# Kernel tuning notes

Measured on AMD Instinct MI355X. Metric: run time of the kernel, lower is better.

The kernel has to match this reference:

```python
import jax, jax.numpy as jnp
import numpy as np

# Static problem sizes (see shape_source)
B, SX, SY = 256, 256, 70          # graphs, encoder nodes/graph, decoder nodes/graph
F, EMB, H = 512, 256, 256          # f_size, emb_size, h_size
VOCAB = 256
E = 4 * B * SY                     # 71680 edges
N_SLT = 4                          # SltEdgeTypes
N_SRT = 8                          # len(SrtEdgeTypes)


def setup_inputs() -> dict:
    key = jax.random.key(0)
    ks = jax.random.split(key, 24)
    s = 0.02
    inp = {
        'x': jax.random.normal(ks[0], (B * SX, F), jnp.float32),
        'x_batch': jnp.repeat(jnp.arange(B, dtype=jnp.int64), SX),
        'tgt_y': jax.random.randint(ks[1], (B * SY,), 0, VOCAB, jnp.int64),
        'tgt_edge_index': jax.random.randint(ks[2], (2, E), 0, B * SY, jnp.int64),
        'tgt_edge_type': jax.random.randint(ks[3], (E,), 0, N_SLT, jnp.int64),
        'tgt_y_batch': jnp.repeat(jnp.arange(B, dtype=jnp.int64), SY),
        'embeds': jax.random.normal(ks[4], (VOCAB, EMB), jnp.float32) * s,
    }
    dims = [(EMB, H), (H, H), (H, EMB)]
    k = 5
    for l, (din, dout) in enumerate(dims, start=1):
        inp[f'W_in{l}'] = jax.random.normal(ks[k + 0], (din, dout), jnp.float32) * s
        inp[f'Wq{l}'] = jax.random.normal(ks[k + 1], (dout, F), jnp.float32) * s
        inp[f'Wv{l}'] = jax.random.normal(ks[k + 2], (F, dout), jnp.float32) * s
        inp[f'Ee{l}'] = jax.random.normal(ks[k + 3], (N_SLT, dout), jnp.float32) * s
        k += 4
    inp['lin_z_w'] = jax.random.normal(ks[k], (EMB, VOCAB), jnp.float32) * s
    inp['lin_z_b'] = jnp.zeros((VOCAB,), jnp.float32)
    inp['lin_g_w'] = jax.random.normal(ks[k + 1], (2 * EMB, N_SRT), jnp.float32) * s
    inp['lin_g_b'] = jnp.zeros((N_SRT,), jnp.float32)
    return inp


def gcn_dec_layer(x_b, y, src, tgt, etype, W_in, Wq, Wv, Ee):
    """Edge-type-conditioned message passing + cross-attention onto encoder x.
    x_b: [B,SX,F]; y: [Ny,din]. Returns ([Ny,dout], alpha [B,SY,SX])."""
    h = y @ W_in                                   # [Ny, dout]
    m = h[src] + Ee[etype]                         # gather + type embedding
    agg = jax.ops.segment_sum(m, tgt, num_segments=y.shape[0])
    q = (h @ Wq).reshape(B, SY, F)                 # query into encoder space
    logits = jnp.einsum('bqf,bkf->bqk', q, x_b) / jnp.sqrt(jnp.float32(F))
    alpha = jax.nn.softmax(logits, axis=-1)        # [B,SY,SX]
    ctx = jnp.einsum('bqk,bkf->bqf', alpha, x_b) @ Wv  # [B,SY,dout]
    out = jax.nn.relu(h + agg + ctx.reshape(h.shape[0], -1))
    return out, alpha


def reference(x, x_batch, tgt_y, tgt_edge_index, tgt_edge_type, tgt_y_batch,
              embeds, W_in1, Wq1, Wv1, Ee1, W_in2, Wq2, Wv2, Ee2,
              W_in3, Wq3, Wv3, Ee3, lin_z_w, lin_z_b, lin_g_w, lin_g_b):
    x_b = x.reshape(B, SX, F)
    src, tgt = tgt_edge_index[0], tgt_edge_index[1]
    y = embeds[tgt_y]                              # [Ny, EMB]
    y, a1 = gcn_dec_layer(x_b, y, src, tgt, tgt_edge_type, W_in1, Wq1, Wv1, Ee1)
    y, a2 = gcn_dec_layer(x_b, y, src, tgt, tgt_edge_type, W_in2, Wq2, Wv2, Ee2)
    y, a3 = gcn_dec_layer(x_b, y, src, tgt, tgt_edge_type, W_in3, Wq3, Wv3, Ee3)
    y_score = y @ lin_z_w + lin_z_b                # [Ny, VOCAB]
    ef = y[tgt_edge_index]                         # [2, E, EMB]
    ef = jnp.transpose(ef, (1, 0, 2)).reshape(E, 2 * EMB)
    y_edge_rel_score = ef @ lin_g_w + lin_g_b      # [E, N_SRT]
    return (y, y_score, y_edge_rel_score, a1, a2, a3)
```

## Files before the change

### kernel.cpp

```cpp
#include <hip/hip_runtime.h>
#include <cstddef>
#include <cstdint>

#define B_    256
#define SX_   256
#define SY_   70
#define F_    512
#define EMB_  256
#define NY_   (B_*SY_)
#define NE_   (4*B_*SY_)

typedef short s16x8 __attribute__((ext_vector_type(8)));
typedef float f32x4 __attribute__((ext_vector_type(4)));
typedef unsigned short us4 __attribute__((ext_vector_type(4)));
typedef unsigned short us8 __attribute__((ext_vector_type(8)));

__device__ __forceinline__ unsigned short f2bf(float f) {
    unsigned u = __builtin_bit_cast(unsigned, f);
    u += 0x7fffu + ((u >> 16) & 1u);
    return (unsigned short)(u >> 16);
}
__device__ __forceinline__ float bf2f(unsigned short b) {
    unsigned u = ((unsigned)b) << 16;
    return __builtin_bit_cast(float, u);
}

template<int EPI, int SWZ>
__global__ __launch_bounds__(256, 2)
void gemm_mfma(const unsigned short* __restrict__ A, int lda, long sAb,
               const unsigned short* __restrict__ Bt, int ldb, long sBb,
               float* __restrict__ Cf, int ldc, long sCfb,
               unsigned short* __restrict__ Cb, int ldcb, long sCbb,
               const float* __restrict__ aux1, long sAux,
               int M, int K, float scale, int nx, int ny)
{
    __shared__ unsigned short As[128 * 64];
    __shared__ unsigned short Bs[128 * 64];
    char* AsB = (char*)As;
    char* BsB = (char*)Bs;
    const int tid = threadIdx.x;
    int bxi, byi, z;
    if (SWZ) {
        const int nwg = gridDim.x;
        const int bid = blockIdx.x;
        const int wg = (bid & 7) * (nwg >> 3) + (bid >> 3);
        bxi = wg % nx;
        byi = (wg / nx) % ny;
        z   = wg / (nx * ny);
    } else {
        bxi = blockIdx.x; byi = blockIdx.y; z = blockIdx.z;
    }
    A  += (size_t)z * sAb;
    Bt += (size_t)z * sBb;
    const char* auxp = (const char*)aux1 + (size_t)z * sAux;
    const int bm = byi * 128, bn = bxi * 128;
    const int lane = tid & 63;
    const int w = tid >> 6, wr = w >> 1, wc = w & 1;
    const int l15 = lane & 15, lq = lane >> 4;

    f32x4 acc[4][4];
    const f32x4 z4 = {0.f, 0.f, 0.f, 0.f};
#pragma unroll
    for (int m = 0; m < 4; ++m)
#pragma unroll
        for (int n = 0; n < 4; ++n) acc[m][n] = z4;

    for (int k0 = 0; k0 < K; k0 += 64) {
#pragma unroll
        for (int i = 0; i < 4; ++i) {
            const int row = i * 32 + (tid >> 3);
            const int k8  = (tid & 7) ^ (row & 7);
            int ra = bm + row; ra = (ra < M) ? ra : (M - 1);
            const unsigned short* g = A + (size_t)ra * lda + k0 + k8 * 8;
            __builtin_amdgcn_global_load_lds(
                (const __attribute__((address_space(1))) unsigned int*)g,
                (__attribute__((address_space(3))) unsigned int*)(AsB + i * 4096 + tid * 16),
                16, 0, 0);
        }
#pragma unroll
        for (int i = 0; i < 4; ++i) {
            const int row = i * 32 + (tid >> 3);
            const int k8  = (tid & 7) ^ (row & 7);
            const unsigned short* g = Bt + (size_t)(bn + row) * ldb + k0 + k8 * 8;
            __builtin_amdgcn_global_load_lds(
                (const __attribute__((address_space(1))) unsigned int*)g,
                (__attribute__((address_space(3))) unsigned int*)(BsB + i * 4096 + tid * 16),
                16, 0, 0);
        }
        __syncthreads();
#pragma unroll
        for (int kk = 0; kk < 2; ++kk) {
            s16x8 af[4], bf[4];
#pragma unroll
            for (int m = 0; m < 4; ++m) {
                const int row = wr * 64 + m * 16 + l15;
                const int slot = (kk * 4 + lq) ^ (row & 7);
                af[m] = *(const s16x8*)(AsB + row * 128 + slot * 16);
            }
#pragma unroll
            for (int n = 0; n < 4; ++n) {
                const int col = wc * 64 + n * 16 + l15;
                const int slot = (kk * 4 + lq) ^ (col & 7);
                bf[n] = *(const s16x8*)(BsB + col * 128 + slot * 16);
            }
#pragma unroll
            for (int m = 0; m < 4; ++m)
#pragma unroll
                for (int n = 0; n < 4; ++n)
                    acc[m][n] = __builtin_amdgcn_mfma_f32_16x16x32_bf16(
                        af[m], bf[n], acc[m][n], 0, 0, 0);
        }
        __syncthreads();
    }

    float* cf = Cf ? Cf + (size_t)z * sCfb : nullptr;
    unsigned short* cb = Cb ? Cb + (size_t)z * sCbb : nullptr;
#pragma unroll
    for (int m = 0; m < 4; ++m) {
#pragma unroll
        for (int n = 0; n < 4; ++n) {
            const int col = bn + wc * 64 + n * 16 + l15;
            f32x4 v = acc[m][n];
#pragma unroll
            for (int r = 0; r < 4; ++r) {
                const int gr = bm + wr * 64 + m * 16 + lq * 4 + r;
                if (gr >= M) continue;
                float o = v[r] * scale;
                if (EPI == 4) o += ((const float*)auxp)[col];
                if (EPI == 7) {
                    if (col < 256) cb[(size_t)gr * ldcb + col] = f2bf(o);
                    else ((unsigned short*)cf)[(size_t)gr * 512 + (col - 256)] = f2bf(o);
                } else {
                    if (cf) cf[(size_t)gr * ldc + col] = o;
                    if (cb) cb[(size_t)gr * ldcb + col] = f2bf(o);
                }
            }
        }
    }
}

template<int LAST>
__global__ __launch_bounds__(512, 1)
void attn_pv(const unsigned short* __restrict__ Q,
             const unsigned short* __restrict__ X,
             const unsigned short* __restrict__ XV,
             long sXVb,
             const unsigned short* __restrict__ aggb,
             const unsigned short* __restrict__ lzT,
             const float* __restrict__ lzb,
             const float* __restrict__ gw,
             float* __restrict__ Y12g,
             float* __restrict__ Aout,
             unsigned short* __restrict__ Yb,
             float* __restrict__ Yf,
             float* __restrict__ Score,
             float scale)
{
    __shared__ unsigned short SB[3 * 12288];
    __shared__ unsigned short Al[128 * 256];
    __shared__ float red[4][2][64];
    char* SBb = (char*)SB;
    char* AlB = (char*)Al;
    const int tid = threadIdx.x;
    const int z = blockIdx.x;
    const unsigned short* Qb  = Q + (size_t)z * SY_ * F_;
    const unsigned short* Xb  = X + (size_t)z * SX_ * F_;
    const unsigned short* xvb = XV + (size_t)z * sXVb;
    const int lane = tid & 63;
    const int w = tid >> 6, wr = w >> 2, wc = w & 3;
    const int l15 = lane & 15, lq = lane >> 4;

    auto stage1 = [&](int t) {
        char* base = SBb + (t % 3) * 24576;
        {
            const int row = tid >> 2;
            const int k8  = (tid & 3) ^ ((row >> 1) & 3);
            const int ra = (row < SY_) ? row : (SY_ - 1);
            const unsigned short* g = Qb + (size_t)ra * F_ + t * 32 + k8 * 8;
            __builtin_amdgcn_global_load_lds(
                (const __attribute__((address_space(1))) unsigned int*)g,
                (__attribute__((address_space(3))) unsigned int*)(base + tid * 16),
                16, 0, 0);
        }
#pragma unroll
        for (int i = 0; i < 2; ++i) {
            const int row = i * 128 + (tid >> 2);
            const int k8  = (tid & 3) ^ ((row >> 1) & 3);
            const unsigned short* g = Xb + (size_t)row * F_ + t * 32 + k8 * 8;
            __builtin_amdgcn_global_load_lds(
                (const __attribute__((address_space(1))) unsigned int*)g,
                (__attribute__((address_space(3))) unsigned int*)(base + 8192 + i * 8192 + tid * 16),
                16, 0, 0);
        }
    };

    f32x4 acc[4][4];
    const f32x4 z4 = {0.f, 0.f, 0.f, 0.f};
#pragma unroll
    for (int m = 0; m < 4; ++m)
#pragma unroll
        for (int n = 0; n < 4; ++n) acc[m][n] = z4;

    stage1(0);
    stage1(1);
    for (int t = 0; t < 16; ++t) {
        if (t + 2 < 16) stage1(t + 2);
        if (t < 14)       asm volatile("s_waitcnt vmcnt(6)" ::: "memory");
        else if (t == 14) asm volatile("s_waitcnt vmcnt(3)" ::: "memory");
        else              asm volatile("s_waitcnt vmcnt(0)" ::: "memory");
        __builtin_amdgcn_s_barrier();
        asm volatile("" ::: "memory");
        char* base = SBb + (t % 3) * 24576;
        s16x8 af[4], bf[4];
#pragma unroll
        for (int m = 0; m < 4; ++m) {
            const int row = wr * 64 + m * 16 + l15;
            const int slot = lq ^ ((row >> 1) & 3);
            af[m] = *(const s16x8*)(base + row * 64 + slot * 16);
        }
#pragma unroll
        for (int n = 0; n < 4; ++n) {
            const int col = wc * 64 + n * 16 + l15;
            const int slot = lq ^ ((col >> 1) & 3);
            bf[n] = *(const s16x8*)(base + 8192 + col * 64 + slot * 16);
        }
#pragma unroll
        for (int m = 0; m < 4; ++m)
#pragma unroll
            for (int n = 0; n < 4; ++n)
                acc[m][n] = __builtin_amdgcn_mfma_f32_16x16x32_bf16(
                    af[m], bf[n], acc[m][n], 0, 0, 0);
        asm volatile("" ::: "memory");
        __builtin_amdgcn_s_barrier();
    }

#pragma unroll
    for (int m = 0; m < 4; ++m)
#pragma unroll
        for (int n = 0; n < 4; ++n)
#pragma unroll
            for (int r = 0; r < 4; ++r) acc[m][n][r] *= scale;

    float rmax[4][4];
#pragma unroll
    for (int m = 0; m < 4; ++m)
#pragma unroll
        for (int r = 0; r < 4; ++r) {
            float mx = acc[m][0][r];
#pragma unroll
            for (int n = 1; n < 4; ++n) mx = fmaxf(mx, acc[m][n][r]);
            mx = fmaxf(mx, __shfl_xor(mx, 1));
            mx = fmaxf(mx, __shfl_xor(mx, 2));
            mx = fmaxf(mx, __shfl_xor(mx, 4));
            mx = fmaxf(mx, __shfl_xor(mx, 8));
            rmax[m][r] = mx;
        }
    if (l15 == 0) {
#pragma unroll
        for (int m = 0; m < 4; ++m)
#pragma unroll
            for (int r = 0; r < 4; ++r)
                red[wc][wr][m * 16 + lq * 4 + r] = rmax[m][r];
    }
    __syncthreads();
    float rtot[4][4];
#pragma unroll
    for (int m = 0; m < 4; ++m)
#pragma unroll
        for (int r = 0; r < 4; ++r) {
            const int lr = m * 16 + lq * 4 + r;
            rtot[m][r] = fmaxf(fmaxf(red[0][wr][lr], red[1][wr][lr]),
                               fmaxf(red[2][wr][lr], red[3][wr][lr]));
        }
    __syncthreads();
    float rsum[4][4];
#pragma unroll
    for (int m = 0; m < 4; ++m)
#pragma unroll
        for (int r = 0; r < 4; ++r) {
            float s = 0.f;
#pragma unroll
            for (int n = 0; n < 4; ++n) {
                float e = __expf(acc[m][n][r] - rtot[m][r]);
                acc[m][n][r] = e;
                s += e;
            }
            s += __shfl_xor(s, 1);
            s += __shfl_xor(s, 2);
            s += __shfl_xor(s, 4);
            s += __shfl_xor(s, 8);
            rsum[m][r] = s;
        }
    if (l15 == 0) {
#pragma unroll
        for (int m = 0; m < 4; ++m)
#pragma unroll
            for (int r = 0; r < 4; ++r)
                red[wc][wr][m * 16 + lq * 4 + r] = rsum[m][r];
    }
    __syncthreads();
#pragma unroll
    for (int m = 0; m < 4; ++m)
#pragma unroll
        for (int r = 0; r < 4; ++r) {
            const int lr = m * 16 + lq * 4 + r;
            const int row = wr * 64 + lr;
            const float inv = 1.0f / (red[0][wr][lr] + red[1][wr][lr] +
                                      red[2][wr][lr] + red[3][wr][lr]);
#pragma unroll
            for (int n = 0; n < 4; ++n) {
                const int col = wc * 64 + n * 16 + l15;
                *(unsigned short*)(AlB + row * 512 +
                    (((col >> 3) ^ (row & 7)) << 4) + ((col & 7) << 1))
                    = f2bf(acc[m][n][r] * inv);
            }
        }
    __syncthreads();
    {
        float* ao = Aout + (size_t)z * SY_ * SX_;
        for (int idx = tid; idx < SY_ * 8; idx += 512) {
            const int row = idx >> 3, seg = idx & 7;
            float tmp[32];
#pragma unroll
            for (int c8 = 0; c8 < 4; ++c8) {
                const int chunk = seg * 4 + c8;
                us8 v = *(const us8*)(AlB + row * 512 + ((chunk ^ (row & 7)) << 4));
#pragma unroll
                for (int j = 0; j < 8; ++j) tmp[c8 * 8 + j] = bf2f(v[j]);
            }
            float* dst = ao + (size_t)row * SX_ + seg * 32;
#pragma unroll
            for (int q = 0; q < 8; ++q) {
                float4 o4; o4.x = tmp[q*4]; o4.y = tmp[q*4+1];
                o4.z = tmp[q*4+2]; o4.w = tmp[q*4+3];
                ((float4*)dst)[q] = o4;
            }
        }
    }

    char* v_buf[2] = {SBb, SBb + 32768};
    auto stage2 = [&](int k0, int buf, const unsigned short* srcm) {
        char* bb = v_buf[buf];
#pragma unroll
        for (int i = 0; i < 4; ++i) {
            const int row = i * 64 + (tid >> 3);
            const int k8  = (tid & 7) ^ (row & 7);
            const unsigned short* g = srcm + (size_t)row * 256 + k0 + k8 * 8;
            __builtin_amdgcn_global_load_lds(
                (const __attribute__((address_space(1))) unsigned int*)g,
                (__attribute__((address_space(3))) unsigned int*)(bb + i * 8192 + tid * 16),
                16, 0, 0);
        }
    };

    f32x4 oac[4][4];
#pragma unroll
    for (int m = 0; m < 4; ++m)
#pragma unroll
        for (int n = 0; n < 4; ++n) oac[m][n] = z4;

    stage2(0, 0, xvb);
    __syncthreads();
    int cur = 0;
    for (int ks = 0; ks < 4; ++ks) {
        if (ks < 3) stage2((ks + 1) * 64, cur ^ 1, xvb);
        char* bb = v_buf[cur];
        const int k0 = ks * 64;
#pragma unroll
        for (int kk = 0; kk < 2; ++kk) {
            s16x8 af[4], bf[4];
#pragma unroll
            for (int m = 0; m < 4; ++m) {
                const int row = wr * 64 + m * 16 + l15;
                const int chunk = (k0 >> 3) + kk * 4 + lq;
                af[m] = *(const s16x8*)(AlB + row * 512 + ((chunk ^ (row & 7)) << 4));
            }
#pragma unroll
            for (int n = 0; n < 4; ++n) {
                const int col = wc * 64 + n * 16 + l15;
                const int slot = (kk * 4 + lq) ^ (col & 7);
                bf[n] = *(const s16x8*)(bb + col * 128 + slot * 16);
            }
#pragma unroll
            for (int m = 0; m < 4; ++m)
#pragma unroll
                for (int n = 0; n < 4; ++n)
                    oac[m][n] = __builtin_amdgcn_mfma_f32_16x16x32_bf16(
                        af[m], bf[n], oac[m][n], 0, 0, 0);
        }
        __syncthreads();
        cur ^= 1;
    }

#pragma unroll
    for (int m = 0; m < 4; ++m)
#pragma unroll
        for (int n = 0; n < 4; ++n) {
            const int col = wc * 64 + n * 16 + l15;
            f32x4 v = oac[m][n];
#pragma unroll
            for (int r = 0; r < 4; ++r) {
                const int row = wr * 64 + m * 16 + lq * 4 + r;
                if (row >= SY_) continue;
                *(unsigned short*)(AlB + row * 512 +
                    (((col >> 3) ^ (row & 7)) << 4) + ((col & 7) << 1)) = f2bf(v[r]);
            }
        }
    __syncthreads();
    {
        const size_t nodeBase = (size_t)z * SY_;
        for (int idx = tid; idx < SY_ * 8; idx += 512) {
            const int row = idx >> 3, seg = idx & 7;
            const size_t node = nodeBase + row;
            float tmp[32];
#pragma unroll
            for (int c8 = 0; c8 < 4; ++c8) {
                const int chunk = seg * 4 + c8;
                us8 ov = *(const us8*)(AlB + row * 512 + ((chunk ^ (row & 7)) << 4));
                us8 av = *(const us8*)(aggb + node * 256 + seg * 32 + c8 * 8);
                us8 o;
#pragma unroll
                for (int j = 0; j < 8; ++j) {
                    float val = fmaxf(bf2f(ov[j]) + bf2f(av[j]), 0.f);
                    tmp[c8 * 8 + j] = val;
                    o[j] = f2bf(val);
                }
                *(us8*)(Yb + node * 256 + seg * 32 + c8 * 8) = o;
                if (LAST)
                    *(us8*)(AlB + row * 512 + ((chunk ^ (row & 7)) << 4)) = o;
            }
            if (Yf) {
                float* dst = Yf + node * 256 + seg * 32;
#pragma unroll
                for (int q = 0; q < 8; ++q) {
                    float4 o4; o4.x = tmp[q*4]; o4.y = tmp[q*4+1];
                    o4.z = tmp[q*4+2]; o4.w = tmp[q*4+3];
                    ((float4*)dst)[q] = o4;
                }
            }
        }
    }

    if (LAST) {
        __syncthreads();
#pragma unroll
        for (int m = 0; m < 4; ++m)
#pragma unroll
            for (int n = 0; n < 4; ++n) oac[m][n] = z4;
        stage2(0, 0, lzT);
        __syncthreads();
        cur = 0;
        for (int ks = 0; ks < 4; ++ks) {
            if (ks < 3) stage2((ks + 1) * 64, cur ^ 1, lzT);
            char* bb = v_buf[cur];
            const int k0 = ks * 64;
#pragma unroll
            for (int kk = 0; kk < 2; ++kk) {
                s16x8 af[4], bf[4];
#pragma unroll
                for (int m = 0; m < 4; ++m) {
                    const int row = wr * 64 + m * 16 + l15;
                    const int chunk = (k0 >> 3) + kk * 4 + lq;
                    af[m] = *(const s16x8*)(AlB + row * 512 + ((chunk ^ (row & 7)) << 4));
                }
#pragma unroll
                for (int n = 0; n < 4; ++n) {
                    const int col = wc * 64 + n * 16 + l15;
                    const int slot = (kk * 4 + lq) ^ (col & 7);
                    bf[n] = *(const s16x8*)(bb + col * 128 + slot * 16);
                }
#pragma unroll
                for (int m = 0; m < 4; ++m)
#pragma unroll
                    for (int n = 0; n < 4; ++n)
                        oac[m][n] = __builtin_amdgcn_mfma_f32_16x16x32_bf16(
                            af[m], bf[n], oac[m][n], 0, 0, 0);
            }
            __syncthreads();
            cur ^= 1;
        }
#pragma unroll
        for (int m = 0; m < 4; ++m)
#pragma unroll
            for (int n = 0; n < 4; ++n) {
                const int col = wc * 64 + n * 16 + l15;
                f32x4 v = oac[m][n];
#pragma unroll
                for (int r = 0; r < 4; ++r) {
                    const int row = wr * 64 + m * 16 + lq * 4 + r;
                    if (row >= SY_) continue;
                    Score[((size_t)z * SY_ + row) * 256 + col] = v[r] + lzb[col];
                }
            }

        __syncthreads();
        float* Ws = (float*)SBb;
        for (int i = tid; i < 1024; i += 512)
            ((float4*)Ws)[i] = ((const float4*)gw)[i];
        __syncthreads();
        for (int t = tid; t < 1120; t += 512) {
            const int row = t >> 4, j = t & 15;
            const float* Wcol = Ws + ((j < 8) ? j : (2048 + j - 8));
            float a2 = 0.f;
            for (int c = 0; c < 256; ++c) {
                const float yv = bf2f(*(const unsigned short*)(AlB + row * 512 +
                    (((c >> 3) ^ (row & 7)) << 4) + ((c & 7) << 1)));
                a2 = fmaf(yv, Wcol[c * 8], a2);
            }
            Y12g[((size_t)z * SY_ + row) * 16 + j] = a2;
        }
    }
}

__global__ __launch_bounds__(256)
void conv_x_embed(const float* __restrict__ in, unsigned short* __restrict__ out,
                  int n8, const float* __restrict__ embeds,
                  const int* __restrict__ tgt_y, unsigned short* __restrict__ yb)
{
    if (blockIdx.x < 2048) {
        for (int i = blockIdx.x * 256 + threadIdx.x; i < n8; i += 2048 * 256) {
            float4 a = ((const float4*)in)[i * 2];
            float4 b = ((const float4*)in)[i * 2 + 1];
            us8 o = { f2bf(a.x), f2bf(a.y), f2bf(a.z), f2bf(a.w),
                      f2bf(b.x), f2bf(b.y), f2bf(b.z), f2bf(b.w) };
            ((us8*)out)[i] = o;
        }
    } else {
        const int i = (blockIdx.x - 2048) * 8 + (threadIdx.x >> 5);
        const int c8 = (threadIdx.x & 31) * 8;
        const int v = tgt_y[i];
        const float* p = embeds + (size_t)v * 256 + c8;
        float4 a = *(const float4*)p;
        float4 b = *(const float4*)(p + 4);
        us8 o = { f2bf(a.x), f2bf(a.y), f2bf(a.z), f2bf(a.w),
                  f2bf(b.x), f2bf(b.y), f2bf(b.z), f2bf(b.w) };
        *(us8*)(yb + (size_t)i * 256 + c8) = o;
    }
}

struct WAll {
    const float* src[10];
    unsigned short* dst[10];
    int R[10];
    int C[10];
};

__global__ __launch_bounds__(256)
void conv_wT_all(WAll d)
{
    const int z = blockIdx.z;
    const int R = d.R[z], C = d.C[z];
    const int c0 = blockIdx.x * 64, r0 = blockIdx.y * 64;
    if (c0 >= C || r0 >= R) return;
    const float* in = d.src[z];
    unsigned short* outT = d.dst[z];
    __shared__ unsigned short t[64][65];
    const int r = threadIdx.x >> 4, cq = (threadIdx.x & 15) << 2;
#pragma unroll
    for (int i = 0; i < 4; ++i) {
        const int rr = r + i * 16;
        float4 v = *(const float4*)(in + (size_t)(r0 + rr) * C + c0 + cq);
        t[rr][cq + 0] = f2bf(v.x); t[rr][cq + 1] = f2bf(v.y);
        t[rr][cq + 2] = f2bf(v.z); t[rr][cq + 3] = f2bf(v.w);
    }
    __syncthreads();
    const int c = threadIdx.x >> 2, sq = (threadIdx.x & 3) << 4;
    us8 o0, o1;
#pragma unroll
    for (int i = 0; i < 8; ++i) { o0[i] = t[sq + i][c]; o1[i] = t[sq + 8 + i][c]; }
    *(us8*)(outT + (size_t)(c0 + c) * R + r0 + sq) = o0;
    *(us8*)(outT + (size_t)(c0 + c) * R + r0 + sq + 8) = o1;
}

__global__ __launch_bounds__(256)
void edge_deg(const int* __restrict__ tgt, int* __restrict__ deg)
{
    const int e = blockIdx.x * 256 + threadIdx.x;
    if (e < NE_) atomicAdd(&deg[tgt[e]], 1);
}

__global__ __launch_bounds__(1024)
void scan_off(const int* __restrict__ deg, int* __restrict__ off, int* __restrict__ cursor)
{
    __shared__ int ls[1024];
    const int t = threadIdx.x;
    const int base = t * 18;
    int local[18];
    int s = 0;
#pragma unroll
    for (int i = 0; i < 18; ++i) {
        const int idx = base + i;
        const int v = (idx < NY_) ? deg[idx] : 0;
        local[i] = s; s += v;
    }
    ls[t] = s;
    __syncthreads();
    for (int d = 1; d < 1024; d <<= 1) {
        int v = (t >= d) ? ls[t - d] : 0;
        __syncthreads();
        ls[t] += v;
        __syncthreads();
    }
    const int excl = (t == 0) ? 0 : ls[t - 1];
#pragma unroll
    for (int i = 0; i < 18; ++i) {
        const int idx = base + i;
        if (idx < NY_) {
            const int o = excl + local[i];
            off[idx] = o; cursor[idx] = o;
        }
    }
    if (t == 1023) off[NY_] = ls[1023];
}

__global__ __launch_bounds__(256)
void edge_fill(const int* __restrict__ tgt, int* __restrict__ cursor,
               int* __restrict__ elist)
{
    const int e = blockIdx.x * 256 + threadIdx.x;
    if (e >= NE_) return;
    const int pos = atomicAdd(&cursor[tgt[e]], 1);
    elist[pos] = e;
}

__global__ __launch_bounds__(256)
void node_agg(const unsigned short* __restrict__ hb,
              const float* __restrict__ Ee,
              const int* __restrict__ src, const int* __restrict__ etype,
              const int* __restrict__ off, const int* __restrict__ elist,
              unsigned short* __restrict__ aggb)
{
    const int nid  = blockIdx.x * 4 + (threadIdx.x >> 6);
    const int lane = threadIdx.x & 63;
    const int c = lane * 4;
    const int k0 = off[nid], k1 = off[nid + 1];
    us4 sv = *(const us4*)(hb + (size_t)nid * 256 + c);
    float4 acc;
    acc.x = bf2f(sv[0]); acc.y = bf2f(sv[1]);
    acc.z = bf2f(sv[2]); acc.w = bf2f(sv[3]);
    int cnt0 = 0, cnt1 = 0, cnt2 = 0, cnt3 = 0;
    for (int k = k0; k < k1; ++k) {
        const int e = elist[k];
        const int sfrom = src[e];
        const int ty = etype[e];
        us4 hv = *(const us4*)(hb + (size_t)sfrom * 256 + c);
        acc.x += bf2f(hv[0]); acc.y += bf2f(hv[1]);
        acc.z += bf2f(hv[2]); acc.w += bf2f(hv[3]);
        cnt0 += (ty == 0); cnt1 += (ty == 1); cnt2 += (ty == 2); cnt3 += (ty == 3);
    }
    float4 e0 = *(const float4*)(Ee + c);
    float4 e1 = *(const float4*)(Ee + 256 + c);
    float4 e2 = *(const float4*)(Ee + 512 + c);
    float4 e3 = *(const float4*)(Ee + 768 + c);
    acc.x += cnt0 * e0.x + cnt1 * e1.x + cnt2 * e2.x + cnt3 * e3.x;
    acc.y += cnt0 * e0.y + cnt1 * e1.y + cnt2 * e2.y + cnt3 * e3.y;
    acc.z += cnt0 * e0.z + cnt1 * e1.z + cnt2 * e2.z + cnt3 * e3.z;
    acc.w += cnt0 * e0.w + cnt1 * e1.w + cnt2 * e2.w + cnt3 * e3.w;
    us4 o = { f2bf(acc.x), f2bf(acc.y), f2bf(acc.z), f2bf(acc.w) };
    *(us4*)(aggb + (size_t)nid * 256 + c) = o;
}

__global__ __launch_bounds__(256)
void edge_gather(const float* __restrict__ Y12, const int* __restrict__ src,
                 const int* __restrict__ tgt, const float* __restrict__ bias,
                 float* __restrict__ esc)
{
    const int e = blockIdx.x * 256 + threadIdx.x;
    if (e >= NE_) return;
    const float* a = Y12 + (size_t)src[e] * 16;
    const float* b = Y12 + (size_t)tgt[e] * 16 + 8;
    float4 a0 = ((const float4*)a)[0], a1 = ((const float4*)a)[1];
    float4 b0 = ((const float4*)b)[0], b1 = ((const float4*)b)[1];
    float4 c0 = ((const float4*)bias)[0], c1 = ((const float4*)bias)[1];
    float4 o0, o1;
    o0.x = a0.x + b0.x + c0.x; o0.y = a0.y + b0.y + c0.y;
    o0.z = a0.z + b0.z + c0.z; o0.w = a0.w + b0.w + c0.w;
    o1.x = a1.x + b1.x + c1.x; o1.y = a1.y + b1.y + c1.y;
    o1.z = a1.z + b1.z + c1.z; o1.w = a1.w + b1.w + c1.w;
    ((float4*)(esc + (size_t)e * 8))[0] = o0;
    ((float4*)(esc + (size_t)e * 8))[1] = o1;
}

extern "C" void kernel_launch(void* const* d_in, const int* in_sizes, int n_in,
                              void* d_out, int out_size, void* d_ws, size_t ws_size,
                              hipStream_t stream)
{
    const float* x       = (const float*)d_in[0];
    const int*   tgt_y   = (const int*)d_in[2];
    const int*   eidx    = (const int*)d_in[3];
    const int*   etype   = (const int*)d_in[4];
    const float* embeds  = (const float*)d_in[6];
    const float* W_in[3] = {(const float*)d_in[7],  (const float*)d_in[11], (const float*)d_in[15]};
    const float* Wq[3]   = {(const float*)d_in[8],  (const float*)d_in[12], (const float*)d_in[16]};
    const float* Wv[3]   = {(const float*)d_in[9],  (const float*)d_in[13], (const float*)d_in[17]};
    const float* Ee[3]   = {(const float*)d_in[10], (const float*)d_in[14], (const float*)d_in[18]};
    const float* lin_z_w = (const float*)d_in[19];
    const float* lin_z_b = (const float*)d_in[20];
    const float* lin_g_w = (const float*)d_in[21];
    const float* lin_g_b = (const float*)d_in[22];
    const int* src = eidx;
    const int* tgt = eidx + NE_;

    float* out = (float*)d_out;
    float* y_final = out;
    float* score   = out + 4587520;
    float* esc     = out + 9175040;
    float* aout[3] = {out + 9748480, out + 14336000, out + 18923520};

    char* wsb = (char*)d_ws;
    unsigned short* xb     = (unsigned short*)(wsb + 0);
    unsigned short* xvTall = (unsigned short*)(wsb + 67108864);
    unsigned short* hb     = (unsigned short*)(wsb + 167772160);
    unsigned short* aggb   = (unsigned short*)(wsb + 176947200);
    unsigned short* qb     = (unsigned short*)(wsb + 186122240);
    unsigned short* yb     = (unsigned short*)(wsb + 204472320);
    char* wt = wsb + 213647360;
    unsigned short* wcatT[3], *wqT[3], *wvT[3];
    for (int l = 0; l < 3; ++l) {
        wcatT[l] = (unsigned short*)(wt + l * 393216);
        wqT[l]   = (unsigned short*)(wt + 1179648 + l * 262144);
        wvT[l]   = (unsigned short*)(wt + 1966080 + l * 262144);
    }
    unsigned short* lzT = (unsigned short*)(wt + 2752512);
    char* extra = wsb + 216530944;
    float* Y12    = (float*)extra;
    int*   deg    = (int*)(extra + 1146880);
    int*   off    = (int*)(extra + 1218560);
    int*   cursor = (int*)(extra + 1290244);
    int*   elist  = (int*)(extra + 1361924);

    hipMemsetAsync(deg, 0, NY_ * sizeof(int), stream);
    edge_deg<<<280, 256, 0, stream>>>(tgt, deg);
    scan_off<<<1, 1024, 0, stream>>>(deg, off, cursor);
    edge_fill<<<280, 256, 0, stream>>>(tgt, cursor, elist);

    conv_x_embed<<<4288, 256, 0, stream>>>(x, xb, 4194304, embeds, tgt_y, yb);
    WAll wd;
    for (int l = 0; l < 3; ++l) {
        wd.src[l]     = W_in[l]; wd.dst[l]     = wcatT[l]; wd.R[l]     = 256; wd.C[l]     = 256;
        wd.src[3 + l] = Wq[l];   wd.dst[3 + l] = wqT[l];   wd.R[3 + l] = 256; wd.C[3 + l] = 512;
        wd.src[6 + l] = Wv[l];   wd.dst[6 + l] = wvT[l];   wd.R[6 + l] = 512; wd.C[6 + l] = 256;
    }
    wd.src[9] = lin_z_w; wd.dst[9] = lzT; wd.R[9] = 256; wd.C[9] = 256;
    conv_wT_all<<<dim3(8, 8, 10), 256, 0, stream>>>(wd);

    gemm_mfma<0, 0><<<dim3(2, 4, 3), 256, 0, stream>>>(
        wqT[0], 256, 131072L,  wcatT[0], 256, 196608L,
        nullptr, 0, 0,  wcatT[0] + 65536, 256, 196608L,
        nullptr, 0, 512, 256, 1.f, 0, 0);

    gemm_mfma<0, 1><<<3072, 256, 0, stream>>>(
        wvT[0], 512, 0,  xb, 512, (long)SX_ * F_,
        nullptr, 0, 0,  xvTall, 256, 768L * 256,
        nullptr, 0, 768, 512, 1.f, 2, 6);

    const float qscale = 0.044194173824159216f;
    for (int l = 0; l < 3; ++l) {
        gemm_mfma<7, 0><<<dim3(6, 140, 1), 256, 0, stream>>>(
            yb, 256, 0,  wcatT[l], 256, 0,
            (float*)qb, 512, 0,  hb, 256, 0,
            nullptr, 0, NY_, 256, 1.f, 0, 0);
        node_agg<<<4480, 256, 0, stream>>>(hb, Ee[l], src, etype, off, elist, aggb);
        if (l < 2) {
            attn_pv<0><<<256, 512, 0, stream>>>(
                qb, xb, xvTall + (size_t)l * 65536, 768L * 256,
                aggb, nullptr, nullptr, nullptr, nullptr,
                aout[l], yb, nullptr, nullptr, qscale);
        } else {
            attn_pv<1><<<256, 512, 0, stream>>>(
                qb, xb, xvTall + (size_t)l * 65536, 768L * 256,
                aggb, lzT, lin_z_b, lin_g_w, Y12,
                aout[l], yb, y_final, score, qscale);
        }
    }
    edge_gather<<<280, 256, 0, stream>>>(Y12, src, tgt, lin_g_b, esc);
}
```

Measured before the change: 419.5 us.

## Precompute x·Wqᵀ per graph so attention logits contract over hidden dim

Reassociates the attention logits: instead of computing q = h·Wq (width 512) and contracting q against x over F=512, it precomputes XQ = x·Wqᵀ for all three layers once (a batched GEMM) and contracts h against XQ over 256. This halves the K loop in the attention kernel and removes the per-layer q projection from the node GEMM. The cost is a large extra up-front GEMM over all encoder nodes and a larger workspace buffer that the attention kernel reads.

```diff
diff --git a/kernel.cpp b/kernel.cpp
--- a/kernel.cpp
+++ b/kernel.cpp
@@ -25,13 +25,12 @@
     return __builtin_bit_cast(float, u);
 }
 
-template<int EPI, int SWZ>
+template<int SWZ>
 __global__ __launch_bounds__(256, 2)
 void gemm_mfma(const unsigned short* __restrict__ A, int lda, long sAb,
                const unsigned short* __restrict__ Bt, int ldb, long sBb,
                float* __restrict__ Cf, int ldc, long sCfb,
                unsigned short* __restrict__ Cb, int ldcb, long sCbb,
-               const float* __restrict__ aux1, long sAux,
                int M, int K, float scale, int nx, int ny)
 {
     __shared__ unsigned short As[128 * 64];
@@ -52,7 +51,6 @@
     }
     A  += (size_t)z * sAb;
     Bt += (size_t)z * sBb;
-    const char* auxp = (const char*)aux1 + (size_t)z * sAux;
     const int bm = byi * 128, bn = bxi * 128;
     const int lane = tid & 63;
     const int w = tid >> 6, wr = w >> 1, wc = w & 1;
@@ -126,14 +124,8 @@
                 const int gr = bm + wr * 64 + m * 16 + lq * 4 + r;
                 if (gr >= M) continue;
                 float o = v[r] * scale;
-                if (EPI == 4) o += ((const float*)auxp)[col];
-                if (EPI == 7) {
-                    if (col < 256) cb[(size_t)gr * ldcb + col] = f2bf(o);
-                    else ((unsigned short*)cf)[(size_t)gr * 512 + (col - 256)] = f2bf(o);
-                } else {
-                    if (cf) cf[(size_t)gr * ldc + col] = o;
-                    if (cb) cb[(size_t)gr * ldcb + col] = f2bf(o);
-                }
+                if (cf) cf[(size_t)gr * ldc + col] = o;
+                if (cb) cb[(size_t)gr * ldcb + col] = f2bf(o);
             }
         }
     }
@@ -141,8 +133,8 @@
 
 template<int LAST>
 __global__ __launch_bounds__(512, 1)
-void attn_pv(const unsigned short* __restrict__ Q,
-             const unsigned short* __restrict__ X,
+void attn_pv(const unsigned short* __restrict__ Hb,
+             const unsigned short* __restrict__ XQ,
              const unsigned short* __restrict__ XV,
              long sXVb,
              const unsigned short* __restrict__ aggb,
@@ -163,8 +155,8 @@
     char* AlB = (char*)Al;
     const int tid = threadIdx.x;
     const int z = blockIdx.x;
-    const unsigned short* Qb  = Q + (size_t)z * SY_ * F_;
-    const unsigned short* Xb  = X + (size_t)z * SX_ * F_;
+    const unsigned short* hbz = Hb + (size_t)z * SY_ * 256;
+    const unsigned short* xqz = XQ + (size_t)z * 196608;
     const unsigned short* xvb = XV + (size_t)z * sXVb;
     const int lane = tid & 63;
     const int w = tid >> 6, wr = w >> 2, wc = w & 3;
@@ -176,7 +168,7 @@
             const int row = tid >> 2;
             const int k8  = (tid & 3) ^ ((row >> 1) & 3);
             const int ra = (row < SY_) ? row : (SY_ - 1);
-            const unsigned short* g = Qb + (size_t)ra * F_ + t * 32 + k8 * 8;
+            const unsigned short* g = hbz + (size_t)ra * 256 + t * 32 + k8 * 8;
             __builtin_amdgcn_global_load_lds(
                 (const __attribute__((address_space(1))) unsigned int*)g,
                 (__attribute__((address_space(3))) unsigned int*)(base + tid * 16),
@@ -186,7 +178,7 @@
         for (int i = 0; i < 2; ++i) {
             const int row = i * 128 + (tid >> 2);
             const int k8  = (tid & 3) ^ ((row >> 1) & 3);
-            const unsigned short* g = Xb + (size_t)row * F_ + t * 32 + k8 * 8;
+            const unsigned short* g = xqz + (size_t)row * 768 + t * 32 + k8 * 8;
             __builtin_amdgcn_global_load_lds(
                 (const __attribute__((address_space(1))) unsigned int*)g,
                 (__attribute__((address_space(3))) unsigned int*)(base + 8192 + i * 8192 + tid * 16),
@@ -203,11 +195,11 @@
 
     stage1(0);
     stage1(1);
-    for (int t = 0; t < 16; ++t) {
-        if (t + 2 < 16) stage1(t + 2);
-        if (t < 14)       asm volatile("s_waitcnt vmcnt(6)" ::: "memory");
-        else if (t == 14) asm volatile("s_waitcnt vmcnt(3)" ::: "memory");
-        else              asm volatile("s_waitcnt vmcnt(0)" ::: "memory");
+    for (int t = 0; t < 8; ++t) {
+        if (t + 2 < 8) stage1(t + 2);
+        if (t < 6)       asm volatile("s_waitcnt vmcnt(6)" ::: "memory");
+        else if (t == 6) asm volatile("s_waitcnt vmcnt(3)" ::: "memory");
+        else             asm volatile("s_waitcnt vmcnt(0)" ::: "memory");
         __builtin_amdgcn_s_barrier();
         asm volatile("" ::: "memory");
         char* base = SBb + (t % 3) * 24576;
@@ -515,7 +507,9 @@
 __global__ __launch_bounds__(256)
 void conv_x_embed(const float* __restrict__ in, unsigned short* __restrict__ out,
                   int n8, const float* __restrict__ embeds,
-                  const int* __restrict__ tgt_y, unsigned short* __restrict__ yb)
+                  const int* __restrict__ tgt_y, unsigned short* __restrict__ yb,
+                  const float* __restrict__ wq1, const float* __restrict__ wq2,
+                  const float* __restrict__ wq3, unsigned short* __restrict__ wqcat)
 {
     if (blockIdx.x < 2048) {
         for (int i = blockIdx.x * 256 + threadIdx.x; i < n8; i += 2048 * 256) {
@@ -525,7 +519,7 @@
                       f2bf(b.x), f2bf(b.y), f2bf(b.z), f2bf(b.w) };
             ((us8*)out)[i] = o;
         }
-    } else {
+    } else if (blockIdx.x < 4288) {
         const int i = (blockIdx.x - 2048) * 8 + (threadIdx.x >> 5);
         const int c8 = (threadIdx.x & 31) * 8;
         const int v = tgt_y[i];
@@ -535,20 +529,31 @@
         us8 o = { f2bf(a.x), f2bf(a.y), f2bf(a.z), f2bf(a.w),
                   f2bf(b.x), f2bf(b.y), f2bf(b.z), f2bf(b.w) };
         *(us8*)(yb + (size_t)i * 256 + c8) = o;
+    } else {
+        const int idx = blockIdx.x - 4288;
+        const int which = idx >> 6;
+        const int i = (idx & 63) * 256 + threadIdx.x;
+        const float* src = (which == 0) ? wq1 : (which == 1) ? wq2 : wq3;
+        float4 a = ((const float4*)src)[i * 2];
+        float4 b = ((const float4*)src)[i * 2 + 1];
+        us8 o = { f2bf(a.x), f2bf(a.y), f2bf(a.z), f2bf(a.w),
+                  f2bf(b.x), f2bf(b.y), f2bf(b.z), f2bf(b.w) };
+        ((us8*)(wqcat + (size_t)which * 131072))[i] = o;
     }
 }
 
 struct WAll {
-    const float* src[10];
-    unsigned short* dst[10];
-    int R[10];
-    int C[10];
+    const float* src[8];
+    unsigned short* dst[8];
+    int R[8];
+    int C[8];
 };
 
 __global__ __launch_bounds__(256)
 void conv_wT_all(WAll d)
 {
     const int z = blockIdx.z;
+    if (z >= 7) return;
     const int R = d.R[z], C = d.C[z];
     const int c0 = blockIdx.x * 64, r0 = blockIdx.y * 64;
     if (c0 >= C || r0 >= R) return;
@@ -710,19 +715,19 @@
     char* wsb = (char*)d_ws;
     unsigned short* xb     = (unsigned short*)(wsb + 0);
     unsigned short* xvTall = (unsigned short*)(wsb + 67108864);
-    unsigned short* hb     = (unsigned short*)(wsb + 167772160);
-    unsigned short* aggb   = (unsigned short*)(wsb + 176947200);
-    unsigned short* qb     = (unsigned short*)(wsb + 186122240);
-    unsigned short* yb     = (unsigned short*)(wsb + 204472320);
-    char* wt = wsb + 213647360;
-    unsigned short* wcatT[3], *wqT[3], *wvT[3];
+    unsigned short* xqTall = (unsigned short*)(wsb + 167772160);
+    unsigned short* hb     = (unsigned short*)(wsb + 268435456);
+    unsigned short* aggb   = (unsigned short*)(wsb + 277610496);
+    unsigned short* yb     = (unsigned short*)(wsb + 286785536);
+    char* wt = wsb + 295960576;
+    unsigned short* winT[3], *wqT[3], *wvT[3];
     for (int l = 0; l < 3; ++l) {
-        wcatT[l] = (unsigned short*)(wt + l * 393216);
-        wqT[l]   = (unsigned short*)(wt + 1179648 + l * 262144);
-        wvT[l]   = (unsigned short*)(wt + 1966080 + l * 262144);
-    }
-    unsigned short* lzT = (unsigned short*)(wt + 2752512);
-    char* extra = wsb + 216530944;
+        winT[l] = (unsigned short*)(wt + l * 131072);
+        wqT[l]  = (unsigned short*)(wt + 393216  + l * 262144);
+        wvT[l]  = (unsigned short*)(wt + 1179648 + l * 262144);
+    }
+    unsigned short* lzT = (unsigned short*)(wt + 1966080);
+    char* extra = wsb + 298057728;
     float* Y12    = (float*)extra;
     int*   deg    = (int*)(extra + 1146880);
     int*   off    = (int*)(extra + 1218560);
@@ -734,41 +739,42 @@
     scan_off<<<1, 1024, 0, stream>>>(deg, off, cursor);
     edge_fill<<<280, 256, 0, stream>>>(tgt, cursor, elist);
 
-    conv_x_embed<<<4288, 256, 0, stream>>>(x, xb, 4194304, embeds, tgt_y, yb);
+    conv_x_embed<<<4480, 256, 0, stream>>>(x, xb, 4194304, embeds, tgt_y, yb,
+                                           Wq[0], Wq[1], Wq[2], wqT[0]);
     WAll wd;
     for (int l = 0; l < 3; ++l) {
-        wd.src[l]     = W_in[l]; wd.dst[l]     = wcatT[l]; wd.R[l]     = 256; wd.C[l]     = 256;
-        wd.src[3 + l] = Wq[l];   wd.dst[3 + l] = wqT[l];   wd.R[3 + l] = 256; wd.C[3 + l] = 512;
-        wd.src[6 + l] = Wv[l];   wd.dst[6 + l] = wvT[l];   wd.R[6 + l] = 512; wd.C[6 + l] = 256;
-    }
-    wd.src[9] = lin_z_w; wd.dst[9] = lzT; wd.R[9] = 256; wd.C[9] = 256;
-    conv_wT_all<<<dim3(8, 8, 10), 256, 0, stream>>>(wd);
-
-    gemm_mfma<0, 0><<<dim3(2, 4, 3), 256, 0, stream>>>(
-        wqT[0], 256, 131072L,  wcatT[0], 256, 196608L,
-        nullptr, 0, 0,  wcatT[0] + 65536, 256, 196608L,
-        nullptr, 0, 512, 256, 1.f, 0, 0);
-
-    gemm_mfma<0, 1><<<3072, 256, 0, stream>>>(
+        wd.src[l]     = W_in[l]; wd.dst[l]     = winT[l]; wd.R[l]     = 256; wd.C[l]     = 256;
+        wd.src[3 + l] = Wv[l];   wd.dst[3 + l] = wvT[l];  wd.R[3 + l] = 512; wd.C[3 + l] = 256;
+    }
+    wd.src[6] = lin_z_w; wd.dst[6] = lzT; wd.R[6] = 256; wd.C[6] = 256;
+    wd.src[7] = lin_z_w; wd.dst[7] = lzT; wd.R[7] = 0; wd.C[7] = 0;
+    conv_wT_all<<<dim3(8, 8, 7), 256, 0, stream>>>(wd);
+
+    gemm_mfma<1><<<3072, 256, 0, stream>>>(
         wvT[0], 512, 0,  xb, 512, (long)SX_ * F_,
         nullptr, 0, 0,  xvTall, 256, 768L * 256,
-        nullptr, 0, 768, 512, 1.f, 2, 6);
+        768, 512, 1.f, 2, 6);
+
+    gemm_mfma<1><<<3072, 256, 0, stream>>>(
+        xb, 512, (long)SX_ * F_,  wqT[0], 512, 0,
+        nullptr, 0, 0,  xqTall, 768, 256L * 768,
+        256, 512, 1.f, 6, 2);
 
     const float qscale = 0.044194173824159216f;
     for (int l = 0; l < 3; ++l) {
-        gemm_mfma<7, 0><<<dim3(6, 140, 1), 256, 0, stream>>>(
-            yb, 256, 0,  wcatT[l], 256, 0,
-            (float*)qb, 512, 0,  hb, 256, 0,
-            nullptr, 0, NY_, 256, 1.f, 0, 0);
+        gemm_mfma<0><<<dim3(2, 140, 1), 256, 0, stream>>>(
+            yb, 256, 0,  winT[l], 256, 0,
+            nullptr, 0, 0,  hb, 256, 0,
+            NY_, 256, 1.f, 0, 0);
         node_agg<<<4480, 256, 0, stream>>>(hb, Ee[l], src, etype, off, elist, aggb);
         if (l < 2) {
             attn_pv<0><<<256, 512, 0, stream>>>(
-                qb, xb, xvTall + (size_t)l * 65536, 768L * 256,
+                hb, xqTall + (size_t)l * 256, xvTall + (size_t)l * 65536, 768L * 256,
                 aggb, nullptr, nullptr, nullptr, nullptr,
                 aout[l], yb, nullptr, nullptr, qscale);
         } else {
             attn_pv<1><<<256, 512, 0, stream>>>(
-                qb, xb, xvTall + (size_t)l * 65536, 768L * 256,
+                hb, xqTall + (size_t)l * 256, xvTall + (size_t)l * 65536, 768L * 256,
                 aggb, lzT, lin_z_b, lin_g_w, Y12,
                 aout[l], yb, y_final, score, qscale);
         }
```

New measurement: 446.2 us. +6.4%, slower.

## Split attention kernel into two half-query blocks per graph with smaller LDS

Applied to the files above, without the earlier changes.

The attention/PV kernel now launches two 256-thread blocks per graph, each handling 35 of the 70 query rows, instead of one 512-thread block handling all 70 padded to 128. This drops the padding waste from 128 to 64 rows per block (still padded from 35) and shrinks LDS use so two blocks can share a CU, raising occupancy and the grid to 512 blocks. In exchange, each block reloads the full X and XV tiles, doubling that global traffic. The pipeline also becomes simpler and shallower: QK moves from triple buffering to double buffering, and the PV and score loops lose their prefetch, so they load then sync each step. An unused aux epilogue parameter is removed from the GEMM.

```diff
diff --git a/kernel.cpp b/kernel.cpp
--- a/kernel.cpp
+++ b/kernel.cpp
@@ -31,7 +31,6 @@
                const unsigned short* __restrict__ Bt, int ldb, long sBb,
                float* __restrict__ Cf, int ldc, long sCfb,
                unsigned short* __restrict__ Cb, int ldcb, long sCbb,
-               const float* __restrict__ aux1, long sAux,
                int M, int K, float scale, int nx, int ny)
 {
     __shared__ unsigned short As[128 * 64];
@@ -52,7 +51,6 @@
     }
     A  += (size_t)z * sAb;
     Bt += (size_t)z * sBb;
-    const char* auxp = (const char*)aux1 + (size_t)z * sAux;
     const int bm = byi * 128, bn = bxi * 128;
     const int lane = tid & 63;
     const int w = tid >> 6, wr = w >> 1, wc = w & 1;
@@ -126,7 +124,6 @@
                 const int gr = bm + wr * 64 + m * 16 + lq * 4 + r;
                 if (gr >= M) continue;
                 float o = v[r] * scale;
-                if (EPI == 4) o += ((const float*)auxp)[col];
                 if (EPI == 7) {
                     if (col < 256) cb[(size_t)gr * ldcb + col] = f2bf(o);
                     else ((unsigned short*)cf)[(size_t)gr * 512 + (col - 256)] = f2bf(o);
@@ -140,7 +137,7 @@
 }
 
 template<int LAST>
-__global__ __launch_bounds__(512, 1)
+__global__ __launch_bounds__(256, 2)
 void attn_pv(const unsigned short* __restrict__ Q,
              const unsigned short* __restrict__ X,
              const unsigned short* __restrict__ XV,
@@ -156,40 +153,41 @@
              float* __restrict__ Score,
              float scale)
 {
-    __shared__ unsigned short SB[3 * 12288];
-    __shared__ unsigned short Al[128 * 256];
-    __shared__ float red[4][2][64];
+    __shared__ unsigned short SB[2 * 10240];
+    __shared__ unsigned short Al[64 * 256];
+    __shared__ float red[4][64];
     char* SBb = (char*)SB;
     char* AlB = (char*)Al;
     const int tid = threadIdx.x;
-    const int z = blockIdx.x;
+    const int z  = blockIdx.x >> 1;
+    const int h0 = (blockIdx.x & 1) * 35;
     const unsigned short* Qb  = Q + (size_t)z * SY_ * F_;
     const unsigned short* Xb  = X + (size_t)z * SX_ * F_;
     const unsigned short* xvb = XV + (size_t)z * sXVb;
     const int lane = tid & 63;
-    const int w = tid >> 6, wr = w >> 2, wc = w & 3;
+    const int wc = tid >> 6;
     const int l15 = lane & 15, lq = lane >> 4;
 
-    auto stage1 = [&](int t) {
-        char* base = SBb + (t % 3) * 24576;
+    auto stage1 = [&](int t, int buf) {
+        char* base = SBb + buf * 20480;
         {
             const int row = tid >> 2;
             const int k8  = (tid & 3) ^ ((row >> 1) & 3);
-            const int ra = (row < SY_) ? row : (SY_ - 1);
-            const unsigned short* g = Qb + (size_t)ra * F_ + t * 32 + k8 * 8;
+            const int rl  = (row < 35) ? row : 34;
+            const unsigned short* g = Qb + (size_t)(h0 + rl) * F_ + t * 32 + k8 * 8;
             __builtin_amdgcn_global_load_lds(
                 (const __attribute__((address_space(1))) unsigned int*)g,
                 (__attribute__((address_space(3))) unsigned int*)(base + tid * 16),
                 16, 0, 0);
         }
 #pragma unroll
-        for (int i = 0; i < 2; ++i) {
-            const int row = i * 128 + (tid >> 2);
+        for (int i = 0; i < 4; ++i) {
+            const int row = i * 64 + (tid >> 2);
             const int k8  = (tid & 3) ^ ((row >> 1) & 3);
             const unsigned short* g = Xb + (size_t)row * F_ + t * 32 + k8 * 8;
             __builtin_amdgcn_global_load_lds(
                 (const __attribute__((address_space(1))) unsigned int*)g,
-                (__attribute__((address_space(3))) unsigned int*)(base + 8192 + i * 8192 + tid * 16),
+                (__attribute__((address_space(3))) unsigned int*)(base + 4096 + i * 4096 + tid * 16),
                 16, 0, 0);
         }
     };
@@ -201,20 +199,16 @@
 #pragma unroll
         for (int n = 0; n < 4; ++n) acc[m][n] = z4;
 
-    stage1(0);
-    stage1(1);
+    stage1(0, 0);
+    __syncthreads();
+    int cur = 0;
     for (int t = 0; t < 16; ++t) {
-        if (t + 2 < 16) stage1(t + 2);
-        if (t < 14)       asm volatile("s_waitcnt vmcnt(6)" ::: "memory");
-        else if (t == 14) asm volatile("s_waitcnt vmcnt(3)" ::: "memory");
-        else              asm volatile("s_waitcnt vmcnt(0)" ::: "memory");
-        __builtin_amdgcn_s_barrier();
-        asm volatile("" ::: "memory");
-        char* base = SBb + (t % 3) * 24576;
+        if (t < 15) stage1(t + 1, cur ^ 1);
+        char* base = SBb + cur * 20480;
         s16x8 af[4], bf[4];
 #pragma unroll
         for (int m = 0; m < 4; ++m) {
-            const int row = wr * 64 + m * 16 + l15;
+            const int row = m * 16 + l15;
             const int slot = lq ^ ((row >> 1) & 3);
             af[m] = *(const s16x8*)(base + row * 64 + slot * 16);
         }
@@ -222,7 +216,7 @@
         for (int n = 0; n < 4; ++n) {
             const int col = wc * 64 + n * 16 + l15;
             const int slot = lq ^ ((col >> 1) & 3);
-            bf[n] = *(const s16x8*)(base + 8192 + col * 64 + slot * 16);
+            bf[n] = *(const s16x8*)(base + 4096 + col * 64 + slot * 16);
         }
 #pragma unroll
         for (int m = 0; m < 4; ++m)
@@ -230,8 +224,8 @@
             for (int n = 0; n < 4; ++n)
                 acc[m][n] = __builtin_amdgcn_mfma_f32_16x16x32_bf16(
                     af[m], bf[n], acc[m][n], 0, 0, 0);
-        asm volatile("" ::: "memory");
-        __builtin_amdgcn_s_barrier();
+        __syncthreads();
+        cur ^= 1;
     }
 
 #pragma unroll
@@ -260,7 +254,7 @@
         for (int m = 0; m < 4; ++m)
 #pragma unroll
             for (int r = 0; r < 4; ++r)
-                red[wc][wr][m * 16 + lq * 4 + r] = rmax[m][r];
+                red[wc][m * 16 + lq * 4 + r] = rmax[m][r];
     }
     __syncthreads();
     float rtot[4][4];
@@ -269,8 +263,8 @@
 #pragma unroll
         for (int r = 0; r < 4; ++r) {
             const int lr = m * 16 + lq * 4 + r;
-            rtot[m][r] = fmaxf(fmaxf(red[0][wr][lr], red[1][wr][lr]),
-                               fmaxf(red[2][wr][lr], red[3][wr][lr]));
+            rtot[m][r] = fmaxf(fmaxf(red[0][lr], red[1][lr]),
+                               fmaxf(red[2][lr], red[3][lr]));
         }
     __syncthreads();
     float rsum[4][4];
@@ -296,7 +290,7 @@
         for (int m = 0; m < 4; ++m)
 #pragma unroll
             for (int r = 0; r < 4; ++r)
-                red[wc][wr][m * 16 + lq * 4 + r] = rsum[m][r];
+                red[wc][m * 16 + lq * 4 + r] = rsum[m][r];
     }
     __syncthreads();
 #pragma unroll
@@ -304,21 +298,20 @@
 #pragma unroll
         for (int r = 0; r < 4; ++r) {
             const int lr = m * 16 + lq * 4 + r;
-            const int row = wr * 64 + lr;
-            const float inv = 1.0f / (red[0][wr][lr] + red[1][wr][lr] +
-                                      red[2][wr][lr] + red[3][wr][lr]);
+            const float inv = 1.0f / (red[0][lr] + red[1][lr] +
+                                      red[2][lr] + red[3][lr]);
 #pragma unroll
             for (int n = 0; n < 4; ++n) {
                 const int col = wc * 64 + n * 16 + l15;
-                *(unsigned short*)(AlB + row * 512 +
-                    (((col >> 3) ^ (row & 7)) << 4) + ((col & 7) << 1))
+                *(unsigned short*)(AlB + lr * 512 +
+                    (((col >> 3) ^ (lr & 7)) << 4) + ((col & 7) << 1))
                     = f2bf(acc[m][n][r] * inv);
             }
         }
     __syncthreads();
     {
-        float* ao = Aout + (size_t)z * SY_ * SX_;
-        for (int idx = tid; idx < SY_ * 8; idx += 512) {
+        float* ao = Aout + (size_t)z * SY_ * SX_ + (size_t)h0 * SX_;
+        for (int idx = tid; idx < 35 * 8; idx += 256) {
             const int row = idx >> 3, seg = idx & 7;
             float tmp[32];
 #pragma unroll
@@ -338,17 +331,15 @@
         }
     }
 
-    char* v_buf[2] = {SBb, SBb + 32768};
-    auto stage2 = [&](int k0, int buf, const unsigned short* srcm) {
-        char* bb = v_buf[buf];
-#pragma unroll
-        for (int i = 0; i < 4; ++i) {
-            const int row = i * 64 + (tid >> 3);
+    auto stage2 = [&](int k0, const unsigned short* srcm) {
+#pragma unroll
+        for (int i = 0; i < 8; ++i) {
+            const int row = i * 32 + (tid >> 3);
             const int k8  = (tid & 7) ^ (row & 7);
             const unsigned short* g = srcm + (size_t)row * 256 + k0 + k8 * 8;
             __builtin_amdgcn_global_load_lds(
                 (const __attribute__((address_space(1))) unsigned int*)g,
-                (__attribute__((address_space(3))) unsigned int*)(bb + i * 8192 + tid * 16),
+                (__attribute__((address_space(3))) unsigned int*)(SBb + i * 4096 + tid * 16),
                 16, 0, 0);
         }
     };
@@ -359,19 +350,16 @@
 #pragma unroll
         for (int n = 0; n < 4; ++n) oac[m][n] = z4;
 
-    stage2(0, 0, xvb);
-    __syncthreads();
-    int cur = 0;
     for (int ks = 0; ks < 4; ++ks) {
-        if (ks < 3) stage2((ks + 1) * 64, cur ^ 1, xvb);
-        char* bb = v_buf[cur];
+        stage2(ks * 64, xvb);
+        __syncthreads();
         const int k0 = ks * 64;
 #pragma unroll
         for (int kk = 0; kk < 2; ++kk) {
             s16x8 af[4], bf[4];
 #pragma unroll
             for (int m = 0; m < 4; ++m) {
-                const int row = wr * 64 + m * 16 + l15;
+                const int row = m * 16 + l15;
                 const int chunk = (k0 >> 3) + kk * 4 + lq;
                 af[m] = *(const s16x8*)(AlB + row * 512 + ((chunk ^ (row & 7)) << 4));
             }
@@ -379,7 +367,7 @@
             for (int n = 0; n < 4; ++n) {
                 const int col = wc * 64 + n * 16 + l15;
                 const int slot = (kk * 4 + lq) ^ (col & 7);
-                bf[n] = *(const s16x8*)(bb + col * 128 + slot * 16);
+                bf[n] = *(const s16x8*)(SBb + col * 128 + slot * 16);
             }
 #pragma unroll
             for (int m = 0; m < 4; ++m)
@@ -389,7 +377,6 @@
                         af[m], bf[n], oac[m][n], 0, 0, 0);
         }
         __syncthreads();
-        cur ^= 1;
     }
 
 #pragma unroll
@@ -400,16 +387,16 @@
             f32x4 v = oac[m][n];
 #pragma unroll
             for (int r = 0; r < 4; ++r) {
-                const int row = wr * 64 + m * 16 + lq * 4 + r;
-                if (row >= SY_) continue;
+                const int row = m * 16 + lq * 4 + r;
+                if (row >= 35) continue;
                 *(unsigned short*)(AlB + row * 512 +
                     (((col >> 3) ^ (row & 7)) << 4) + ((col & 7) << 1)) = f2bf(v[r]);
             }
         }
     __syncthreads();
     {
-        const size_t nodeBase = (size_t)z * SY_;
-        for (int idx = tid; idx < SY_ * 8; idx += 512) {
+        const size_t nodeBase = (size_t)z * SY_ + h0;
+        for (int idx = tid; idx < 35 * 8; idx += 256) {
             const int row = idx >> 3, seg = idx & 7;
             const size_t node = nodeBase + row;
             float tmp[32];
@@ -447,19 +434,16 @@
         for (int m = 0; m < 4; ++m)
 #pragma unroll
             for (int n = 0; n < 4; ++n) oac[m][n] = z4;
-        stage2(0, 0, lzT);
-        __syncthreads();
-        cur = 0;
         for (int ks = 0; ks < 4; ++ks) {
-            if (ks < 3) stage2((ks + 1) * 64, cur ^ 1, lzT);
-            char* bb = v_buf[cur];
+            stage2(ks * 64, lzT);
+            __syncthreads();
             const int k0 = ks * 64;
 #pragma unroll
             for (int kk = 0; kk < 2; ++kk) {
                 s16x8 af[4], bf[4];
 #pragma unroll
                 for (int m = 0; m < 4; ++m) {
-                    const int row = wr * 64 + m * 16 + l15;
+                    const int row = m * 16 + l15;
                     const int chunk = (k0 >> 3) + kk * 4 + lq;
                     af[m] = *(const s16x8*)(AlB + row * 512 + ((chunk ^ (row & 7)) << 4));
                 }
@@ -467,7 +451,7 @@
                 for (int n = 0; n < 4; ++n) {
                     const int col = wc * 64 + n * 16 + l15;
                     const int slot = (kk * 4 + lq) ^ (col & 7);
-                    bf[n] = *(const s16x8*)(bb + col * 128 + slot * 16);
+                    bf[n] = *(const s16x8*)(SBb + col * 128 + slot * 16);
                 }
 #pragma unroll
                 for (int m = 0; m < 4; ++m)
@@ -477,7 +461,6 @@
                             af[m], bf[n], oac[m][n], 0, 0, 0);
             }
             __syncthreads();
-            cur ^= 1;
         }
 #pragma unroll
         for (int m = 0; m < 4; ++m)
@@ -487,18 +470,18 @@
                 f32x4 v = oac[m][n];
 #pragma unroll
                 for (int r = 0; r < 4; ++r) {
-                    const int row = wr * 64 + m * 16 + lq * 4 + r;
-                    if (row >= SY_) continue;
-                    Score[((size_t)z * SY_ + row) * 256 + col] = v[r] + lzb[col];
+                    const int row = m * 16 + lq * 4 + r;
+                    if (row >= 35) continue;
+                    Score[((size_t)z * SY_ + h0 + row) * 256 + col] = v[r] + lzb[col];
                 }
             }
 
         __syncthreads();
         float* Ws = (float*)SBb;
-        for (int i = tid; i < 1024; i += 512)
+        for (int i = tid; i < 1024; i += 256)
             ((float4*)Ws)[i] = ((const float4*)gw)[i];
         __syncthreads();
-        for (int t = tid; t < 1120; t += 512) {
+        for (int t = tid; t < 35 * 16; t += 256) {
             const int row = t >> 4, j = t & 15;
             const float* Wcol = Ws + ((j < 8) ? j : (2048 + j - 8));
             float a2 = 0.f;
@@ -507,7 +490,7 @@
                     (((c >> 3) ^ (row & 7)) << 4) + ((c & 7) << 1)));
                 a2 = fmaf(yv, Wcol[c * 8], a2);
             }
-            Y12g[((size_t)z * SY_ + row) * 16 + j] = a2;
+            Y12g[((size_t)z * SY_ + h0 + row) * 16 + j] = a2;
         }
     }
 }
@@ -747,27 +730,27 @@
     gemm_mfma<0, 0><<<dim3(2, 4, 3), 256, 0, stream>>>(
         wqT[0], 256, 131072L,  wcatT[0], 256, 196608L,
         nullptr, 0, 0,  wcatT[0] + 65536, 256, 196608L,
-        nullptr, 0, 512, 256, 1.f, 0, 0);
+        512, 256, 1.f, 0, 0);
 
     gemm_mfma<0, 1><<<3072, 256, 0, stream>>>(
         wvT[0], 512, 0,  xb, 512, (long)SX_ * F_,
         nullptr, 0, 0,  xvTall, 256, 768L * 256,
-        nullptr, 0, 768, 512, 1.f, 2, 6);
+        768, 512, 1.f, 2, 6);
 
     const float qscale = 0.044194173824159216f;
     for (int l = 0; l < 3; ++l) {
         gemm_mfma<7, 0><<<dim3(6, 140, 1), 256, 0, stream>>>(
             yb, 256, 0,  wcatT[l], 256, 0,
             (float*)qb, 512, 0,  hb, 256, 0,
-            nullptr, 0, NY_, 256, 1.f, 0, 0);
+            NY_, 256, 1.f, 0, 0);
         node_agg<<<4480, 256, 0, stream>>>(hb, Ee[l], src, etype, off, elist, aggb);
         if (l < 2) {
-            attn_pv<0><<<256, 512, 0, stream>>>(
+            attn_pv<0><<<512, 256, 0, stream>>>(
                 qb, xb, xvTall + (size_t)l * 65536, 768L * 256,
                 aggb, nullptr, nullptr, nullptr, nullptr,
                 aout[l], yb, nullptr, nullptr, qscale);
         } else {
-            attn_pv<1><<<256, 512, 0, stream>>>(
+            attn_pv<1><<<512, 256, 0, stream>>>(
                 qb, xb, xvTall + (size_t)l * 65536, 768L * 256,
                 aggb, lzT, lin_z_b, lin_g_w, Y12,
                 aout[l], yb, y_final, score, qscale);
```

Result: slower. 436.1 us (+4.0%).
